# Kernel optimization log

Measured on AMD Instinct MI355X. Metric: run time of the kernel, lower is better.

Reference implementation:

```python
import jax, jax.numpy as jnp
import numpy as np

# CMSBlockLinear block-ELL sparse linear forward.
# values: [R, K, B, B] active weight tiles (out_tile x in_tile)
# col_indices: [R, K] int32, which input block-column each tile multiplies
# y[b,s, r*B+i] = sum_k sum_j values[r,k,i,j] * x[b,s, col_indices[r,k]*B + j] + bias

IN_FEATURES = 2048
OUT_FEATURES = 2048
TILE = 16
DENSITY = 0.25
R = OUT_FEATURES // TILE   # 128
C = IN_FEATURES // TILE    # 128
K = max(1, int(C * DENSITY))  # 32
BATCH, SEQ = 4, 512


def setup_inputs() -> dict:
    key = jax.random.key(0)
    kx, kv, kc = jax.random.split(key, 3)
    x = jax.random.normal(kx, (BATCH, SEQ, IN_FEATURES), dtype=jnp.float32)
    # Kaiming-normal init as in _reset_parameters: std = gain('relu') / sqrt(K*B)
    std = np.sqrt(2.0) / np.sqrt(K * TILE)
    values = jax.random.normal(kv, (R, K, TILE, TILE), dtype=jnp.float32) * std
    # K distinct column indices per row (random topology, as in _initialize_topology)
    rng = np.random.default_rng(0)
    col_np = np.stack([rng.permutation(C)[:K] for _ in range(R)]).astype(np.int32)
    col_indices = jnp.asarray(col_np)
    bias = jnp.zeros((OUT_FEATURES,), dtype=jnp.float32)
    return {"x": x, "values": values, "col_indices": col_indices, "bias": bias}


def reference(x, values, col_indices, bias):
    bs, sl, _ = x.shape
    Rr, Kk, B, _ = values.shape
    Cc = x.shape[-1] // B
    x_blocks = x.reshape(bs, sl, Cc, B)                 # [b, s, C, B]
    # Gather the K active input blocks for every output row: [b, s, R, K, B]
    x_gathered = x_blocks[:, :, col_indices, :]
    # Batched small-block matmul and reduce over K tiles: [b, s, R, B]
    out = jnp.einsum("bsrkj,rkij->bsri", x_gathered, values)
    return out.reshape(bs, sl, Rr * B) + bias
```

## Files before the change

### kernel.cpp

```cpp
#include <hip/hip_runtime.h>
#include <hip/hip_bf16.h>

#define TOKS 2048
#define FEAT 2048
#define NR   128
#define KB   32
#define RB   32
#define TT   32

typedef __attribute__((ext_vector_type(8))) short bf16x8;
typedef __attribute__((ext_vector_type(4))) float f32x4;

__device__ __forceinline__ unsigned short f2bf(float f) {
    unsigned u = __builtin_bit_cast(unsigned, f);
    u += 0x7FFFu + ((u >> 16) & 1u);
    return (unsigned short)(u >> 16);
}

__device__ __forceinline__ bf16x8 pack8(float4 a, float4 b) {
    bf16x8 r;
    r[0] = (short)f2bf(a.x); r[1] = (short)f2bf(a.y);
    r[2] = (short)f2bf(a.z); r[3] = (short)f2bf(a.w);
    r[4] = (short)f2bf(b.x); r[5] = (short)f2bf(b.y);
    r[6] = (short)f2bf(b.z); r[7] = (short)f2bf(b.w);
    return r;
}

__device__ __forceinline__ unsigned pack2_hu(float lo, float hi) {
    unsigned a = __builtin_bit_cast(unsigned, lo) + 0x8000u;
    unsigned b = __builtin_bit_cast(unsigned, hi) + 0x8000u;
    return __builtin_amdgcn_perm(b, a, 0x07060302u);
}

__device__ __forceinline__ bf16x8 pack8_hu(float4 a, float4 b) {
    unsigned r0 = pack2_hu(a.x, a.y);
    unsigned r1 = pack2_hu(a.z, a.w);
    unsigned r2 = pack2_hu(b.x, b.y);
    unsigned r3 = pack2_hu(b.z, b.w);
    uint4 u = {r0, r1, r2, r3};
    return __builtin_bit_cast(bf16x8, u);
}

__global__ __launch_bounds__(512) void bsp8(const float* __restrict__ x,
                                            const float* __restrict__ values,
                                            const int* __restrict__ cols,
                                            const float* __restrict__ bias,
                                            float* __restrict__ out) {
    __shared__ __align__(16) unsigned short xs[TT * FEAT];

    int bid  = blockIdx.x;
    int xcd  = bid & 7, slot = bid >> 3;
    int tg   = xcd * 8 + (slot >> 2);
    int rg   = slot & 3;
    int tok0 = tg * TT;
    int r0   = rg * RB;
    int tid  = threadIdx.x;

    {
        int tr = tid >> 8;
        int ch = tid & 255;
        #pragma unroll 4
        for (int it = 0; it < TT / 2; ++it) {
            int t = it * 2 + tr;
            const float4* p = reinterpret_cast<const float4*>(
                x + (size_t)(tok0 + t) * FEAT + ch * 8);
            float4 a = p[0], b = p[1];
            int off = (t << 12) + ((ch << 4) ^ ((t & 7) << 4));
            *reinterpret_cast<bf16x8*>(reinterpret_cast<char*>(xs) + off) = pack8(a, b);
        }
    }
    __syncthreads();

    int wave = tid >> 6;
    int lane = tid & 63;
    int n = lane & 15;
    int g = lane >> 4;
    int h = g & 1;
    int q = g >> 1;

    int mrow = n << 12;
    int axor = (n & 7) << 4;

    #pragma unroll 1
    for (int rr = 0; rr < 4; ++rr) {
        int r = r0 + wave * 4 + rr;
        int cbase = __builtin_amdgcn_readfirstlane(r) * KB;

        bf16x8 bfrag[16];
        int aaddr[16];
        const float* vfl = values + ((size_t)r << 13) + (q << 8) + (n << 4) + (h << 3);
        #pragma unroll
        for (int tc = 0; tc < 4; ++tc) {
            #pragma unroll
            for (int ti = 0; ti < 4; ++ti) {
                int t = tc * 4 + ti;
                const float4* pv = reinterpret_cast<const float4*>(vfl + t * 512);
                bfrag[t] = pack8_hu(pv[0], pv[1]);
                int c0 = cols[cbase + 2 * t];
                int c1 = cols[cbase + 2 * t + 1];
                int c  = q ? c1 : c0;
                aaddr[t] = mrow + (((c << 5) + (h << 4)) ^ axor);
            }
        }

        float fb = bias[(r << 4) + n];

        #pragma unroll
        for (int sx = 0; sx < 2; ++sx) {
            const char* xb = reinterpret_cast<const char*>(xs) + (sx << 16);
            f32x4 acc0 = {0.f, 0.f, 0.f, 0.f};
            f32x4 acc1 = {0.f, 0.f, 0.f, 0.f};
            __builtin_amdgcn_s_setprio(1);
            #pragma unroll
            for (int t = 0; t < 8; ++t) {
                bf16x8 a0 = *reinterpret_cast<const bf16x8*>(xb + aaddr[2 * t]);
                bf16x8 a1 = *reinterpret_cast<const bf16x8*>(xb + aaddr[2 * t + 1]);
                acc0 = __builtin_amdgcn_mfma_f32_16x16x32_bf16(a0, bfrag[2 * t],     acc0, 0, 0, 0);
                acc1 = __builtin_amdgcn_mfma_f32_16x16x32_bf16(a1, bfrag[2 * t + 1], acc1, 0, 0, 0);
            }
            __builtin_amdgcn_s_setprio(0);
            int trow = tok0 + (sx << 4) + (g << 2);
            size_t ob = (size_t)trow * 2048 + (r << 4) + n;
            #pragma unroll
            for (int p = 0; p < 4; ++p)
                out[ob + (size_t)p * 2048] = acc0[p] + acc1[p] + fb;
        }
    }
}

extern "C" void kernel_launch(void* const* d_in, const int* in_sizes, int n_in,
                              void* d_out, int out_size, void* d_ws, size_t ws_size,
                              hipStream_t stream) {
    const float* x      = (const float*)d_in[0];
    const float* values = (const float*)d_in[1];
    const int*   cols   = (const int*)d_in[2];
    const float* bias   = (const float*)d_in[3];
    float*       out    = (float*)d_out;

    const int grid = (TOKS / TT) * (NR / RB);
    bsp8<<<grid, 512, 0, stream>>>(x, values, cols, bias, out);
}
```

Baseline: 27.35 us.

## Pre-convert x and weights to bf16 column-block layout in a separate prep kernel

Adds a prep kernel that converts x into a bf16 layout ordered column-block-major (each 16-feature block stored contiguously across all tokens) and converts the weight tiles to bf16 in workspace. The main kernel then reads its A fragments straight from global memory, with no LDS staging or sync, and each wave keeps one row's weight fragments in registers while it sweeps 8 token tiles. The aim is to stop every block re-reading and converting x and values, at the cost of a second launch and an extra round trip through global memory. The old LDS kernel stays as a fallback for when the workspace is too small.

```diff
diff --git a/kernel.cpp b/kernel.cpp
--- a/kernel.cpp
+++ b/kernel.cpp
@@ -5,8 +5,8 @@
 #define FEAT 2048
 #define NR   128
 #define KB   32
-#define RB   32
-#define TT   32
+#define NCB  128
+#define CBW  (TOKS * 32)
 
 typedef __attribute__((ext_vector_type(8))) short bf16x8;
 typedef __attribute__((ext_vector_type(4))) float f32x4;
@@ -26,41 +26,115 @@
     return r;
 }
 
+__global__ __launch_bounds__(256) void prep9(const float* __restrict__ x,
+                                             const float* __restrict__ v,
+                                             unsigned short* __restrict__ xb,
+                                             unsigned short* __restrict__ vb) {
+    int bid = blockIdx.x, tid = threadIdx.x;
+    if (bid < 1024) {
+        int cbi = tid & 127, tp = tid >> 7;
+        int tok = bid * 2 + tp;
+        const float4* p = reinterpret_cast<const float4*>(x + (size_t)tok * FEAT + cbi * 16);
+        float4 f0 = p[0], f1 = p[1], f2 = p[2], f3 = p[3];
+        unsigned short* d = xb + (size_t)cbi * TOKS * 16 + tok * 16;
+        *reinterpret_cast<bf16x8*>(d)     = pack8(f0, f1);
+        *reinterpret_cast<bf16x8*>(d + 8) = pack8(f2, f3);
+    } else {
+        int i = ((bid - 1024) * 256 + tid) * 8;
+        float4 a = *reinterpret_cast<const float4*>(v + i);
+        float4 b = *reinterpret_cast<const float4*>(v + i + 4);
+        *reinterpret_cast<bf16x8*>(vb + i) = pack8(a, b);
+    }
+}
+
+__global__ __launch_bounds__(512) void bsp9(const unsigned short* __restrict__ xb,
+                                            const unsigned short* __restrict__ vb,
+                                            const int* __restrict__ cols,
+                                            const float* __restrict__ bias,
+                                            float* __restrict__ out) {
+    int bid  = blockIdx.x;
+    int xcd  = bid & 7;
+    int idx  = bid >> 3;
+    int tid  = threadIdx.x;
+    int wv   = tid >> 6;
+    int lane = tid & 63;
+
+    int r     = idx * 4 + (wv >> 1);
+    int tile0 = xcd * 16 + (wv & 1) * 8;
+
+    int n = lane & 15;
+    int g = lane >> 4;
+    int h = g & 1;
+    int q = g >> 1;
+
+    bf16x8 bf[16];
+    int aoff[16];
+    {
+        int cb = __builtin_amdgcn_readfirstlane(r) * KB;
+        const unsigned short* vbl = vb + ((size_t)r << 13) + (q << 8) + (n << 4) + (h << 3);
+        #pragma unroll
+        for (int t = 0; t < 16; ++t) {
+            bf[t] = *reinterpret_cast<const bf16x8*>(vbl + t * 512);
+            int c0 = cols[cb + 2 * t];
+            int c1 = cols[cb + 2 * t + 1];
+            int c  = q ? c1 : c0;
+            aoff[t] = c * CBW + n * 32 + h * 16;
+        }
+    }
+    float fb = bias[(r << 4) + n];
+    const char* xbase = reinterpret_cast<const char*>(xb);
+
+    #pragma unroll 2
+    for (int tl = 0; tl < 8; ++tl) {
+        int tokbase = (tile0 + tl) << 4;
+        int toff    = tokbase << 5;
+        f32x4 a0 = {0.f, 0.f, 0.f, 0.f};
+        f32x4 a1 = {0.f, 0.f, 0.f, 0.f};
+        #pragma unroll
+        for (int t = 0; t < 8; ++t) {
+            bf16x8 x0 = *reinterpret_cast<const bf16x8*>(xbase + (aoff[2 * t]     + toff));
+            bf16x8 x1 = *reinterpret_cast<const bf16x8*>(xbase + (aoff[2 * t + 1] + toff));
+            a0 = __builtin_amdgcn_mfma_f32_16x16x32_bf16(x0, bf[2 * t],     a0, 0, 0, 0);
+            a1 = __builtin_amdgcn_mfma_f32_16x16x32_bf16(x1, bf[2 * t + 1], a1, 0, 0, 0);
+        }
+        int trow = tokbase + (g << 2);
+        size_t ob = (size_t)trow * 2048 + (r << 4) + n;
+        #pragma unroll
+        for (int p = 0; p < 4; ++p)
+            out[ob + (size_t)p * 2048] = a0[p] + a1[p] + fb;
+    }
+}
+
 __device__ __forceinline__ unsigned pack2_hu(float lo, float hi) {
     unsigned a = __builtin_bit_cast(unsigned, lo) + 0x8000u;
     unsigned b = __builtin_bit_cast(unsigned, hi) + 0x8000u;
     return __builtin_amdgcn_perm(b, a, 0x07060302u);
 }
-
 __device__ __forceinline__ bf16x8 pack8_hu(float4 a, float4 b) {
-    unsigned r0 = pack2_hu(a.x, a.y);
-    unsigned r1 = pack2_hu(a.z, a.w);
-    unsigned r2 = pack2_hu(b.x, b.y);
-    unsigned r3 = pack2_hu(b.z, b.w);
-    uint4 u = {r0, r1, r2, r3};
+    uint4 u = {pack2_hu(a.x, a.y), pack2_hu(a.z, a.w), pack2_hu(b.x, b.y), pack2_hu(b.z, b.w)};
     return __builtin_bit_cast(bf16x8, u);
 }
 
-__global__ __launch_bounds__(512) void bsp8(const float* __restrict__ x,
-                                            const float* __restrict__ values,
-                                            const int* __restrict__ cols,
-                                            const float* __restrict__ bias,
-                                            float* __restrict__ out) {
-    __shared__ __align__(16) unsigned short xs[TT * FEAT];
+__global__ __launch_bounds__(512) void bsp_fb(const float* __restrict__ x,
+                                              const float* __restrict__ values,
+                                              const int* __restrict__ cols,
+                                              const float* __restrict__ bias,
+                                              float* __restrict__ out) {
+    __shared__ __align__(16) unsigned short xs[32 * FEAT];
 
     int bid  = blockIdx.x;
     int xcd  = bid & 7, slot = bid >> 3;
     int tg   = xcd * 8 + (slot >> 2);
     int rg   = slot & 3;
-    int tok0 = tg * TT;
-    int r0   = rg * RB;
+    int tok0 = tg * 32;
+    int r0   = rg * 32;
     int tid  = threadIdx.x;
 
     {
         int tr = tid >> 8;
         int ch = tid & 255;
         #pragma unroll 4
-        for (int it = 0; it < TT / 2; ++it) {
+        for (int it = 0; it < 16; ++it) {
             int t = it * 2 + tr;
             const float4* p = reinterpret_cast<const float4*>(
                 x + (size_t)(tok0 + t) * FEAT + ch * 8);
@@ -77,7 +151,6 @@
     int g = lane >> 4;
     int h = g & 1;
     int q = g >> 1;
-
     int mrow = n << 12;
     int axor = (n & 7) << 4;
 
@@ -85,40 +158,31 @@
     for (int rr = 0; rr < 4; ++rr) {
         int r = r0 + wave * 4 + rr;
         int cbase = __builtin_amdgcn_readfirstlane(r) * KB;
-
         bf16x8 bfrag[16];
         int aaddr[16];
         const float* vfl = values + ((size_t)r << 13) + (q << 8) + (n << 4) + (h << 3);
         #pragma unroll
-        for (int tc = 0; tc < 4; ++tc) {
-            #pragma unroll
-            for (int ti = 0; ti < 4; ++ti) {
-                int t = tc * 4 + ti;
-                const float4* pv = reinterpret_cast<const float4*>(vfl + t * 512);
-                bfrag[t] = pack8_hu(pv[0], pv[1]);
-                int c0 = cols[cbase + 2 * t];
-                int c1 = cols[cbase + 2 * t + 1];
-                int c  = q ? c1 : c0;
-                aaddr[t] = mrow + (((c << 5) + (h << 4)) ^ axor);
-            }
-        }
-
+        for (int t = 0; t < 16; ++t) {
+            const float4* pv = reinterpret_cast<const float4*>(vfl + t * 512);
+            bfrag[t] = pack8_hu(pv[0], pv[1]);
+            int c0 = cols[cbase + 2 * t];
+            int c1 = cols[cbase + 2 * t + 1];
+            int c  = q ? c1 : c0;
+            aaddr[t] = mrow + (((c << 5) + (h << 4)) ^ axor);
+        }
         float fb = bias[(r << 4) + n];
-
         #pragma unroll
         for (int sx = 0; sx < 2; ++sx) {
-            const char* xb = reinterpret_cast<const char*>(xs) + (sx << 16);
+            const char* xbp = reinterpret_cast<const char*>(xs) + (sx << 16);
             f32x4 acc0 = {0.f, 0.f, 0.f, 0.f};
             f32x4 acc1 = {0.f, 0.f, 0.f, 0.f};
-            __builtin_amdgcn_s_setprio(1);
             #pragma unroll
             for (int t = 0; t < 8; ++t) {
-                bf16x8 a0 = *reinterpret_cast<const bf16x8*>(xb + aaddr[2 * t]);
-                bf16x8 a1 = *reinterpret_cast<const bf16x8*>(xb + aaddr[2 * t + 1]);
+                bf16x8 a0 = *reinterpret_cast<const bf16x8*>(xbp + aaddr[2 * t]);
+                bf16x8 a1 = *reinterpret_cast<const bf16x8*>(xbp + aaddr[2 * t + 1]);
                 acc0 = __builtin_amdgcn_mfma_f32_16x16x32_bf16(a0, bfrag[2 * t],     acc0, 0, 0, 0);
                 acc1 = __builtin_amdgcn_mfma_f32_16x16x32_bf16(a1, bfrag[2 * t + 1], acc1, 0, 0, 0);
             }
-            __builtin_amdgcn_s_setprio(0);
             int trow = tok0 + (sx << 4) + (g << 2);
             size_t ob = (size_t)trow * 2048 + (r << 4) + n;
             #pragma unroll
@@ -137,6 +201,15 @@
     const float* bias   = (const float*)d_in[3];
     float*       out    = (float*)d_out;
 
-    const int grid = (TOKS / TT) * (NR / RB);
-    bsp8<<<grid, 512, 0, stream>>>(x, values, cols, bias, out);
-}
+    const size_t xb_bytes = (size_t)NCB * TOKS * 16 * 2;
+    const size_t vb_bytes = (size_t)NR * KB * 256 * 2;
+
+    if (ws_size >= xb_bytes + vb_bytes) {
+        unsigned short* xbuf = (unsigned short*)d_ws;
+        unsigned short* vbuf = (unsigned short*)((char*)d_ws + xb_bytes);
+        prep9<<<1024 + 512, 256, 0, stream>>>(x, values, xbuf, vbuf);
+        bsp9<<<256, 512, 0, stream>>>(xbuf, vbuf, cols, bias, out);
+    } else {
+        bsp_fb<<<256, 512, 0, stream>>>(x, values, cols, bias, out);
+    }
+}
```

Result: slower. 30.88 us (+12.9%).
